# Performance work log

Hardware: AMD Instinct MI355X
Metric: run time of the kernel (lower is better)

Reference implementation:

```python
import jax, jax.numpy as jnp
import numpy as np

IN_F, OUT_F, N_CLASSES, HEADS = 512, 64, 40, 4
B, M = 1, 4096
NEG_SLOPE = 0.01  # F.leaky_relu called with default slope (self.alpha unused)


def _xavier(key, shape, gain=1.0):
    fan_in, fan_out = shape[-1], shape[-2] if len(shape) > 1 else shape[-1]
    a = gain * np.sqrt(6.0 / (fan_in + fan_out))
    return jax.random.uniform(key, shape, jnp.float32, -a, a)


def setup_inputs() -> dict:
    key = jax.random.key(0)
    ks = jax.random.split(key, 12)
    h = jax.random.normal(ks[0], (B, M, IN_F), jnp.float32)
    A = jax.random.randint(ks[1], (B, M, M), 0, 2, jnp.int32)
    A = jnp.maximum(A, jnp.eye(M, dtype=jnp.int32)[None])  # self-loops avoid empty softmax rows
    return {
        "h": h,
        "A": A,
        "W1_w": _xavier(ks[2], (OUT_F * HEADS, IN_F)),
        "W1_b": jnp.zeros((OUT_F * HEADS,), jnp.float32),
        "a1": _xavier(ks[3], (HEADS, 2 * OUT_F), gain=1.414),
        "W3_w": _xavier(ks[4], (OUT_F, OUT_F * HEADS)),
        "W3_b": jnp.zeros((OUT_F,), jnp.float32),
        "W2_w": _xavier(ks[5], (OUT_F * HEADS, OUT_F)),
        "W2_b": jnp.zeros((OUT_F * HEADS,), jnp.float32),
        "a2": _xavier(ks[6], (HEADS, 2 * OUT_F)),
        "FL_w": _xavier(ks[7], (N_CLASSES, OUT_F * HEADS)),
        "FL_b": jnp.zeros((N_CLASSES,), jnp.float32),
    }


def _attention_block(h, mask, W_w, W_b, a):
    # h: (b,m,n); mask: (b,m,m) bool; W_w: (heads*out, n); a: (heads, 2*out)
    b, m, _ = h.shape
    Wh = jnp.einsum('bmn,on->bmo', h, W_w) + W_b          # (b,m,heads*out)
    Wh = Wh.reshape(b, m, HEADS, -1)                       # (b,m,h,c)
    c = Wh.shape[-1]
    src = jnp.einsum('bmhc,hc->bmh', Wh, a[:, :c])         # score from edge source i
    dst = jnp.einsum('bmhc,hc->bmh', Wh, a[:, c:])         # score from edge target j
    logits = jax.nn.leaky_relu(src[:, :, None, :] + dst[:, None, :, :], NEG_SLOPE)  # (b,i,j,h)
    logits = jnp.where(mask[..., None], logits, -jnp.inf)
    probs = jax.nn.softmax(logits, axis=2)                 # softmax over neighbors j
    out = jnp.einsum('bijh,bjhc->bihc', probs, Wh)
    return out.reshape(b, m, HEADS * c)


def reference(h, A, W1_w, W1_b, a1, W3_w, W3_b, W2_w, W2_b, a2, FL_w, FL_b):
    mask = A == 1
    x = _attention_block(h, mask, W1_w, W1_b, a1)          # (b,m,heads*out)
    x = jnp.einsum('bmo,po->bmp', x, W3_w) + W3_b          # (b,m,out)
    x = _attention_block(x, mask, W2_w, W2_b, a2)          # (b,m,heads*out)
    out = jnp.einsum('bmo,ko->bmk', x, FL_w) + FL_b        # (b,m,n_classes)
    return (x, out)
```

## Files before the change

### kernel.cpp

```cpp
#include <hip/hip_runtime.h>
#include <hip/hip_bf16.h>

typedef _Float16 f16_t;
typedef unsigned short u16;
typedef unsigned int u32;
typedef float f32x4 __attribute__((ext_vector_type(4)));
typedef f16_t f16x8 __attribute__((ext_vector_type(8)));
typedef u16 u16x8 __attribute__((ext_vector_type(8)));
typedef u16 u16x4 __attribute__((ext_vector_type(4)));

#define MROWS 4096
#define NHEADS 4
#define COUT 64
#define OHF 256
#define NCLS 40
#define LOG2E 1.4426950408889634f
#define PLD 264

static __device__ __forceinline__ u16 f16b(float x) {
    return __builtin_bit_cast(u16, (f16_t)x);
}
static __device__ __forceinline__ float f16f(u16 x) {
    return (float)__builtin_bit_cast(f16_t, x);
}
static __device__ __forceinline__ float dmu_decode(u32 ku) {
    const u32 fb = (ku & 0x80000000u) ? (ku ^ 0x80000000u) : ~ku;
    return __builtin_bit_cast(float, fb);
}

__global__ __launch_bounds__(256) void init_kernel(const int* __restrict__ A,
                                                   u32* __restrict__ AbitsT,
                                                   const float* __restrict__ W1w,
                                                   const float* __restrict__ W1b,
                                                   const float* __restrict__ a1,
                                                   const float* __restrict__ W2w,
                                                   const float* __restrict__ W2b,
                                                   const float* __restrict__ W3w,
                                                   const float* __restrict__ W3b,
                                                   const float* __restrict__ a2,
                                                   float* __restrict__ Cwf,
                                                   float* __restrict__ cbf,
                                                   float* __restrict__ va1,
                                                   float* __restrict__ vc1,
                                                   float* __restrict__ va2,
                                                   float* __restrict__ vc2,
                                                   u32* __restrict__ dmu) {
    __shared__ u32 W[2][128];
    __shared__ float u[8][64];
    const int bx = blockIdx.x, tid = threadIdx.x;
    if (bx < 2048) {
        const int i0 = bx * 2;
        const int lane = tid & 63, wv = tid >> 6;
        for (int t = wv; t < 32; t += 4) {
            const int r = t >> 4, q = t & 15;
            const size_t base = (size_t)(i0 + r) * MROWS + q * 256 + lane;
            const int a0 = A[base];
            const int a1_ = A[base + 64];
            const int a2_ = A[base + 128];
            const int a3 = A[base + 192];
            const unsigned long long b0 = __ballot(a0 != 0);
            const unsigned long long b1 = __ballot(a1_ != 0);
            const unsigned long long b2 = __ballot(a2_ != 0);
            const unsigned long long b3 = __ballot(a3 != 0);
            if (lane == 0) {
                W[r][q * 8 + 0] = (u32)b0;
                W[r][q * 8 + 2] = (u32)b1;
                W[r][q * 8 + 4] = (u32)b2;
                W[r][q * 8 + 6] = (u32)b3;
            } else if (lane == 1) {
                W[r][q * 8 + 1] = (u32)(b0 >> 32);
                W[r][q * 8 + 3] = (u32)(b1 >> 32);
                W[r][q * 8 + 5] = (u32)(b2 >> 32);
                W[r][q * 8 + 7] = (u32)(b3 >> 32);
            }
        }
        __syncthreads();
        {
            const int jw = tid >> 1, r = tid & 1;
            AbitsT[(size_t)jw * MROWS + i0 + r] = W[r][jw];
        }
        return;
    }
    const int bid = bx - 2048;
    if (bid < 256) {
        float acc = 0.f;
        for (int t = 0; t < 64; ++t)
            acc += W2w[bid * 64 + t] * W3w[t * 256 + tid];
        Cwf[bid * 256 + tid] = acc;
        if (tid == 0) {
            float b = 0.f;
            for (int t = 0; t < 64; ++t) b += W2w[bid * 64 + t] * W3b[t];
            cbf[bid] = b + W2b[bid];
        }
    } else if (bid < 258) {
        const int k = (bid - 256) * 256 + tid;
#pragma unroll
        for (int hs = 0; hs < 8; ++hs) {
            const int h = hs >> 1, s = hs & 1;
            float acc = 0.f;
            for (int c = 0; c < COUT; ++c)
                acc += W1w[(size_t)(h * COUT + c) * 512 + k] * a1[h * 128 + s * COUT + c];
            va1[hs * 512 + k] = acc;
        }
        if (bid == 256 && tid == 0) {
            for (int hs = 0; hs < 8; ++hs) {
                const int h = hs >> 1, s = hs & 1;
                float b = 0.f;
                for (int c = 0; c < COUT; ++c) b += W1b[h * COUT + c] * a1[h * 128 + s * COUT + c];
                vc1[hs] = b;
            }
        }
    } else if (bid == 258) {
#pragma unroll
        for (int e = tid * 2; e < tid * 2 + 2; ++e) {
            const int hs = e >> 6, t = e & 63;
            const int h = hs >> 1, s = hs & 1;
            float acc = 0.f;
            for (int c = 0; c < COUT; ++c)
                acc += W2w[(size_t)(h * COUT + c) * 64 + t] * a2[h * 128 + s * COUT + c];
            u[hs][t] = acc;
        }
        __syncthreads();
#pragma unroll
        for (int hs = 0; hs < 8; ++hs) {
            float acc = 0.f;
            for (int t = 0; t < 64; ++t) acc += u[hs][t] * W3w[t * 256 + tid];
            va2[hs * 256 + tid] = acc;
        }
        if (tid == 0) {
            for (int hs = 0; hs < 8; ++hs) {
                const int h = hs >> 1, s = hs & 1;
                float b = 0.f;
                for (int t = 0; t < 64; ++t) b += u[hs][t] * W3b[t];
                for (int c = 0; c < COUT; ++c) b += W2b[h * COUT + c] * a2[h * 128 + s * COUT + c];
                vc2[hs] = b;
            }
        }
    } else {
        if (tid < 8) dmu[tid] = 0u;
    }
}

__global__ __launch_bounds__(256) void proj_kernel(const float* __restrict__ X,
                                                   const float* __restrict__ Bm,
                                                   const float* __restrict__ bias,
                                                   int K,
                                                   u16* __restrict__ WhF,
                                                   const float* __restrict__ va,
                                                   const float* __restrict__ vc,
                                                   float* __restrict__ srcT,
                                                   float* __restrict__ dstT,
                                                   u32* __restrict__ dmu) {
    __shared__ u16 Al[64][40];
    __shared__ u16 Bl[64][40];
    __shared__ u16 Tl[64][72];
    __shared__ float red[16][16][9];
    __shared__ float dred[4][16];
    const int tid = threadIdx.x;
    if (blockIdx.x < 256) {
        const int lane = tid & 63, wv = tid >> 6;
        const int l15 = lane & 15, g = lane >> 4;
        const int m0 = (blockIdx.x & 63) * 64, n0 = (blockIdx.x >> 6) * 64;
        const int r = tid >> 2, c8 = (tid & 3) * 8;
        f32x4 acc[4] = {};
        for (int k0 = 0; k0 < K; k0 += 32) {
            const float4 a0 = *(const float4*)&X[(size_t)(m0 + r) * K + k0 + c8];
            const float4 a1 = *(const float4*)&X[(size_t)(m0 + r) * K + k0 + c8 + 4];
            const float4 b0 = *(const float4*)&Bm[(size_t)(n0 + r) * K + k0 + c8];
            const float4 b1 = *(const float4*)&Bm[(size_t)(n0 + r) * K + k0 + c8 + 4];
            u16x8 av, bv;
            av[0] = f16b(a0.x); av[1] = f16b(a0.y); av[2] = f16b(a0.z); av[3] = f16b(a0.w);
            av[4] = f16b(a1.x); av[5] = f16b(a1.y); av[6] = f16b(a1.z); av[7] = f16b(a1.w);
            bv[0] = f16b(b0.x); bv[1] = f16b(b0.y); bv[2] = f16b(b0.z); bv[3] = f16b(b0.w);
            bv[4] = f16b(b1.x); bv[5] = f16b(b1.y); bv[6] = f16b(b1.z); bv[7] = f16b(b1.w);
            __syncthreads();
            *(u16x8*)&Al[r][c8] = av;
            *(u16x8*)&Bl[r][c8] = bv;
            __syncthreads();
            f16x8 afr = *(const f16x8*)&Al[16 * wv + l15][8 * g];
#pragma unroll
            for (int ni = 0; ni < 4; ++ni) {
                f16x8 bfr = *(const f16x8*)&Bl[16 * ni + l15][8 * g];
                acc[ni] = __builtin_amdgcn_mfma_f32_16x16x32_f16(afr, bfr, acc[ni], 0, 0, 0);
            }
        }
#pragma unroll
        for (int ni = 0; ni < 4; ++ni) {
            const int nl = 16 * ni + l15;
            const float bvs = bias[n0 + nl];
#pragma unroll
            for (int rr = 0; rr < 4; ++rr)
                Tl[nl][16 * wv + 4 * g + rr] = f16b(acc[ni][rr] + bvs);
        }
        __syncthreads();
        const int jb0 = m0 >> 5;
#pragma unroll
        for (int q = 0; q < 2; ++q) {
            const int id = tid + 256 * q;
            const int jb_l = id >> 8, rem = id & 255;
            const int c_l = rem >> 2, gf = rem & 3;
            u16x8 v = *(const u16x8*)&Tl[c_l][32 * jb_l + 8 * gf];
            *(u16x8*)&WhF[(size_t)(((jb0 + jb_l) * 256 + n0 + c_l) * 4 + gf) * 8] = v;
        }
        return;
    }
    const int bs = blockIdx.x - 256;
    const int ii = tid >> 4, ki = tid & 15;
    const int i = bs * 16 + ii;
    const int KS = K >> 4;
    const int k0 = ki * KS;
    float acc[8] = {};
    for (int k = k0; k < k0 + KS; k += 4) {
        const float4 xv = *(const float4*)&X[(size_t)i * K + k];
#pragma unroll
        for (int hs = 0; hs < 8; ++hs) {
            const float4 vv = *(const float4*)&va[(size_t)hs * K + k];
            acc[hs] += xv.x * vv.x + xv.y * vv.y + xv.z * vv.z + xv.w * vv.w;
        }
    }
#pragma unroll
    for (int hs = 0; hs < 8; ++hs) red[ii][ki][hs] = acc[hs];
    __syncthreads();
    if (tid < 128) {
        const int row = tid >> 3, hs = tid & 7, h = hs >> 1;
        float sum = 0.f;
#pragma unroll
        for (int kk = 0; kk < 16; ++kk) sum += red[row][kk][hs];
        const float val = sum + vc[hs];
        const int ig = bs * 16 + row;
        if ((hs & 1) == 0) {
            srcT[h * MROWS + ig] = val;
        } else {
            dstT[h * MROWS + ig] = val;
            dred[h][row] = val;
        }
    }
    __syncthreads();
    if (tid < 4) {
        float m = -3.4e38f;
#pragma unroll
        for (int r = 0; r < 16; ++r) m = fmaxf(m, dred[tid][r]);
        const u32 b = __builtin_bit_cast(u32, m);
        const u32 key = (b & 0x80000000u) ? ~b : (b | 0x80000000u);
        atomicMax(dmu + tid, key);
    }
}

template <int JT>
__global__ __launch_bounds__(512) void attn_kernel(const u16* __restrict__ WhF,
                                                   const float* __restrict__ srcT,
                                                   const float* __restrict__ dstT,
                                                   const u32* __restrict__ AbitsT,
                                                   const u32* __restrict__ dmu,
                                                   u16* __restrict__ partial,
                                                   float* __restrict__ outF) {
    constexpr int J64 = JT * 64;
    __shared__ __align__(16) float GT[8 * J64];
    const int tid = threadIdx.x;
    const int lane = tid & 63, w = tid >> 6;
    const int h = w & 3, half = w >> 2;
    const int l15 = lane & 15, g = lane >> 4;
    const int i0 = blockIdx.x * 64;
    const int chunk = blockIdx.y;
    const int jbase = chunk * J64;

    for (int e = tid; e < 8 * J64; e += 512) {
        const int hb = e / J64;
        const int j = e - hb * J64;
        const float dmhe = dmu_decode(dmu[hb >> 1]);
        const float sc = (hb & 1) ? 0.01f * LOG2E : LOG2E;
        GT[e] = __builtin_amdgcn_exp2f((dstT[(hb >> 1) * MROWS + jbase + j] - dmhe) * sc);
    }

    const float dmh = dmu_decode(dmu[h]);
    float negs_[2], F1_[2], F2_[2];
#pragma unroll
    for (int mi = 0; mi < 2; ++mi) {
        const float s = srcT[h * MROWS + i0 + 32 * half + 16 * mi + l15];
        const float sd = s + dmh;
        const float C = fmaxf(sd, 0.01f * sd);
        negs_[mi] = -s;
        F1_[mi] = __builtin_amdgcn_exp2f((sd - C) * LOG2E);
        F2_[mi] = __builtin_amdgcn_exp2f((0.01f * sd - C) * LOG2E);
    }
    __syncthreads();

    f32x4 acc[2][4] = {};
    f32x4 acc1[2] = {};
    f16x8 ones;
#pragma unroll
    for (int e = 0; e < 8; ++e) ones[e] = (f16_t)1.0f;

    for (int jt = 0; jt < JT; ++jt) {
        const int j0 = jbase + jt * 64;
        f16x8 af[2];
#pragma unroll
        for (int kj = 0; kj < 2; ++kj) {
            const int jk = j0 + 32 * kj + 8 * g;
            const float4 d0 = *(const float4*)&dstT[h * MROWS + jk];
            const float4 d1 = *(const float4*)&dstT[h * MROWS + jk + 4];
            float dv[8] = {d0.x, d0.y, d0.z, d0.w, d1.x, d1.y, d1.z, d1.w};
            const int goff = jt * 64 + 32 * kj + 8 * g;
            const float4 g10 = *(const float4*)&GT[(h * 2) * J64 + goff];
            const float4 g11 = *(const float4*)&GT[(h * 2) * J64 + goff + 4];
            const float4 g20 = *(const float4*)&GT[(h * 2 + 1) * J64 + goff];
            const float4 g21 = *(const float4*)&GT[(h * 2 + 1) * J64 + goff + 4];
            const float G1[8] = {g10.x, g10.y, g10.z, g10.w, g11.x, g11.y, g11.z, g11.w};
            const float G2[8] = {g20.x, g20.y, g20.z, g20.w, g21.x, g21.y, g21.z, g21.w};
#pragma unroll
            for (int mi = 0; mi < 2; ++mi) {
                const int irow = i0 + 32 * half + 16 * mi + l15;
                const u32 word = AbitsT[(size_t)((j0 >> 5) + kj) * MROWS + irow];
                const u32 bits = (word >> (8 * g)) & 0xffu;
                f16x8 a;
#pragma unroll
                for (int e = 0; e < 8; ++e) {
                    const bool pos = dv[e] >= negs_[mi];
                    float wv = (pos ? G1[e] : G2[e]) * (pos ? F1_[mi] : F2_[mi]);
                    wv = ((bits >> e) & 1u) ? wv : 0.f;
                    a[e] = (f16_t)wv;
                }
                af[mi] = a;
            }
            const int jb = (j0 >> 5) + kj;
#pragma unroll
            for (int ni = 0; ni < 4; ++ni) {
                const int c = h * COUT + 16 * ni + l15;
                f16x8 b = *(const f16x8*)&WhF[(size_t)(((jb << 8) + c) * 4 + g) * 8];
                acc[0][ni] = __builtin_amdgcn_mfma_f32_16x16x32_f16(af[0], b, acc[0][ni], 0, 0, 0);
                acc[1][ni] = __builtin_amdgcn_mfma_f32_16x16x32_f16(af[1], b, acc[1][ni], 0, 0, 0);
            }
            acc1[0] = __builtin_amdgcn_mfma_f32_16x16x32_f16(af[0], ones, acc1[0], 0, 0, 0);
            acc1[1] = __builtin_amdgcn_mfma_f32_16x16x32_f16(af[1], ones, acc1[1], 0, 0, 0);
        }
    }

    if (partial) {
        u16* pc = partial + (size_t)chunk * MROWS * PLD;
#pragma unroll
        for (int mi = 0; mi < 2; ++mi) {
#pragma unroll
            for (int ni = 0; ni < 4; ++ni)
#pragma unroll
                for (int rr = 0; rr < 4; ++rr) {
                    const int i = i0 + 32 * half + 16 * mi + 4 * g + rr;
                    pc[(size_t)i * PLD + h * COUT + 16 * ni + l15] = f16b(acc[mi][ni][rr]);
                }
#pragma unroll
            for (int rr = 0; rr < 4; ++rr)
                if (l15 == rr)
                    pc[(size_t)(i0 + 32 * half + 16 * mi + 4 * g + rr) * PLD + 256 + h] =
                        f16b(acc1[mi][rr]);
        }
    } else {
#pragma unroll
        for (int mi = 0; mi < 2; ++mi)
#pragma unroll
            for (int rr = 0; rr < 4; ++rr) {
                const int i = i0 + 32 * half + 16 * mi + 4 * g + rr;
                const float rs = acc1[mi][rr];
#pragma unroll
                for (int ni = 0; ni < 4; ++ni)
                    outF[(size_t)i * OHF + h * COUT + 16 * ni + l15] = acc[mi][ni][rr] / rs;
            }
    }
}

__global__ __launch_bounds__(256) void combine_kernel(const u16* __restrict__ partial,
                                                      int nchunk,
                                                      float* __restrict__ outF,
                                                      const float* __restrict__ FLw,
                                                      const float* __restrict__ FLb,
                                                      float* __restrict__ outL) {
    __shared__ float xrow[256];
    __shared__ float cred[40][4];
    const int i = blockIdx.x, c = threadIdx.x, h = c >> 6;
    float v = 0.f, rs = 0.f;
    for (int ch = 0; ch < nchunk; ++ch) {
        const u16* pc = partial + (size_t)ch * MROWS * PLD + (size_t)i * PLD;
        v += f16f(pc[c]);
        rs += f16f(pc[256 + h]);
    }
    const float r = v / rs;
    outF[(size_t)i * OHF + c] = r;
    if (!FLw) return;
    xrow[c] = r;
    __syncthreads();
    if (c < 160) {
        const int k = c >> 2, seg = c & 3;
        const float* xp = &xrow[seg * 64];
        const float* wp = &FLw[(size_t)k * OHF + seg * 64];
        float a = 0.f;
#pragma unroll
        for (int t = 0; t < 64; t += 4) {
            const float4 x4 = *(const float4*)&xp[t];
            const float4 w4 = *(const float4*)&wp[t];
            a += x4.x * w4.x + x4.y * w4.y + x4.z * w4.z + x4.w * w4.w;
        }
        cred[k][seg] = a;
    }
    __syncthreads();
    if (c < NCLS)
        outL[(size_t)i * NCLS + c] = cred[c][0] + cred[c][1] + cred[c][2] + cred[c][3] + FLb[c];
}

extern "C" void kernel_launch(void* const* d_in, const int* in_sizes, int n_in,
                              void* d_out, int out_size, void* d_ws, size_t ws_size,
                              hipStream_t stream) {
    const float* hIn = (const float*)d_in[0];
    const int*   A   = (const int*)d_in[1];
    const float* W1w = (const float*)d_in[2];
    const float* W1b = (const float*)d_in[3];
    const float* a1  = (const float*)d_in[4];
    const float* W3w = (const float*)d_in[5];
    const float* W3b = (const float*)d_in[6];
    const float* W2w = (const float*)d_in[7];
    const float* W2b = (const float*)d_in[8];
    const float* a2  = (const float*)d_in[9];
    const float* FLw = (const float*)d_in[10];
    const float* FLb = (const float*)d_in[11];
    float* outX = (float*)d_out;
    float* outL = outX + (size_t)MROWS * OHF;

    char* p = (char*)d_ws;
    auto alloc = [&](size_t bytes) { char* q = p; p += (bytes + 255) & ~(size_t)255; return q; };
    u32*   AbitsT = (u32*)alloc((size_t)MROWS * 128 * 4);
    u16*   WhF1  = (u16*)alloc((size_t)OHF * MROWS * 2);
    u16*   WhF2  = (u16*)alloc((size_t)OHF * MROWS * 2);
    float* x1f   = (float*)alloc((size_t)MROWS * OHF * 4);
    float* Cwf   = (float*)alloc((size_t)256 * 256 * 4);
    float* cbf   = (float*)alloc(256 * 4);
    float* va1   = (float*)alloc((size_t)8 * 512 * 4);
    float* vc1   = (float*)alloc(8 * 4);
    float* va2   = (float*)alloc((size_t)8 * 256 * 4);
    float* vc2   = (float*)alloc(8 * 4);
    float* srcT1 = (float*)alloc((size_t)NHEADS * MROWS * 4);
    float* dstT1 = (float*)alloc((size_t)NHEADS * MROWS * 4);
    float* srcT2 = (float*)alloc((size_t)NHEADS * MROWS * 4);
    float* dstT2 = (float*)alloc((size_t)NHEADS * MROWS * 4);
    u32*   dmu   = (u32*)alloc(8 * 4);
    size_t fixed = (size_t)(p - (char*)d_ws);
    int nchunk = 8;
    if (fixed + (size_t)8 * MROWS * PLD * 2 > ws_size) nchunk = 4;
    u16* partial = (u16*)p;

    dim3 blk(256);
    init_kernel<<<dim3(2308), blk, 0, stream>>>(A, AbitsT, W1w, W1b, a1, W2w, W2b,
                                                W3w, W3b, a2, Cwf, cbf, va1, vc1,
                                                va2, vc2, dmu);

    auto launch_attn = [&](const u16* WhF, const float* srcT, const float* dstT,
                           const u32* dm) {
        if (nchunk == 8)
            attn_kernel<8><<<dim3(64, 8), dim3(512), 0, stream>>>(WhF, srcT, dstT, AbitsT, dm, partial, nullptr);
        else
            attn_kernel<16><<<dim3(64, 4), dim3(512), 0, stream>>>(WhF, srcT, dstT, AbitsT, dm, partial, nullptr);
    };

    proj_kernel<<<dim3(512), blk, 0, stream>>>(hIn, W1w, W1b, 512, WhF1,
                                               va1, vc1, srcT1, dstT1, dmu);
    launch_attn(WhF1, srcT1, dstT1, dmu);
    combine_kernel<<<dim3(4096), blk, 0, stream>>>(partial, nchunk, x1f,
                                                   nullptr, nullptr, nullptr);

    proj_kernel<<<dim3(512), blk, 0, stream>>>(x1f, Cwf, cbf, 256, WhF2,
                                               va2, vc2, srcT2, dstT2, dmu + 4);
    launch_attn(WhF2, srcT2, dstT2, dmu + 4);
    combine_kernel<<<dim3(4096), blk, 0, stream>>>(partial, nchunk, outX,
                                                   FLw, FLb, outL);
}
```

Baseline: 181.8 us.

## Replace leaky-relu branch with fmax form and halve rows per attention block

The per-element sign test against the destination score is replaced by fmaxf(G1*F1, G2*F2). Because exp is monotonic, the larger of the two exponentials equals the leaky-relu branch, so the dstT loads and the compare/select work in the inner loop go away. Each block now covers 32 rows instead of 64, with one 16-row MFMA tile per wave, and the grid is doubled. This cuts register pressure and raises block count, but loses reuse of the WhF B-fragments across two row tiles, so those global loads double.

```diff
diff --git a/kernel.cpp b/kernel.cpp
--- a/kernel.cpp
+++ b/kernel.cpp
@@ -258,9 +258,9 @@
     __shared__ __align__(16) float GT[8 * J64];
     const int tid = threadIdx.x;
     const int lane = tid & 63, w = tid >> 6;
-    const int h = w & 3, half = w >> 2;
+    const int h = w & 3, mi = w >> 2;
     const int l15 = lane & 15, g = lane >> 4;
-    const int i0 = blockIdx.x * 64;
+    const int i0 = blockIdx.x * 32;
     const int chunk = blockIdx.y;
     const int jbase = chunk * J64;
 
@@ -273,33 +273,24 @@
     }
 
     const float dmh = dmu_decode(dmu[h]);
-    float negs_[2], F1_[2], F2_[2];
-#pragma unroll
-    for (int mi = 0; mi < 2; ++mi) {
-        const float s = srcT[h * MROWS + i0 + 32 * half + 16 * mi + l15];
-        const float sd = s + dmh;
-        const float C = fmaxf(sd, 0.01f * sd);
-        negs_[mi] = -s;
-        F1_[mi] = __builtin_amdgcn_exp2f((sd - C) * LOG2E);
-        F2_[mi] = __builtin_amdgcn_exp2f((0.01f * sd - C) * LOG2E);
-    }
+    const float s = srcT[h * MROWS + i0 + 16 * mi + l15];
+    const float sd = s + dmh;
+    const float C = fmaxf(sd, 0.01f * sd);
+    const float F1 = __builtin_amdgcn_exp2f((sd - C) * LOG2E);
+    const float F2 = __builtin_amdgcn_exp2f((0.01f * sd - C) * LOG2E);
     __syncthreads();
 
-    f32x4 acc[2][4] = {};
-    f32x4 acc1[2] = {};
+    f32x4 acc[4] = {};
+    f32x4 acc1 = {};
     f16x8 ones;
 #pragma unroll
     for (int e = 0; e < 8; ++e) ones[e] = (f16_t)1.0f;
+    const int irow = i0 + 16 * mi + l15;
 
     for (int jt = 0; jt < JT; ++jt) {
         const int j0 = jbase + jt * 64;
-        f16x8 af[2];
 #pragma unroll
         for (int kj = 0; kj < 2; ++kj) {
-            const int jk = j0 + 32 * kj + 8 * g;
-            const float4 d0 = *(const float4*)&dstT[h * MROWS + jk];
-            const float4 d1 = *(const float4*)&dstT[h * MROWS + jk + 4];
-            float dv[8] = {d0.x, d0.y, d0.z, d0.w, d1.x, d1.y, d1.z, d1.w};
             const int goff = jt * 64 + 32 * kj + 8 * g;
             const float4 g10 = *(const float4*)&GT[(h * 2) * J64 + goff];
             const float4 g11 = *(const float4*)&GT[(h * 2) * J64 + goff + 4];
@@ -307,62 +298,48 @@
             const float4 g21 = *(const float4*)&GT[(h * 2 + 1) * J64 + goff + 4];
             const float G1[8] = {g10.x, g10.y, g10.z, g10.w, g11.x, g11.y, g11.z, g11.w};
             const float G2[8] = {g20.x, g20.y, g20.z, g20.w, g21.x, g21.y, g21.z, g21.w};
-#pragma unroll
-            for (int mi = 0; mi < 2; ++mi) {
-                const int irow = i0 + 32 * half + 16 * mi + l15;
-                const u32 word = AbitsT[(size_t)((j0 >> 5) + kj) * MROWS + irow];
-                const u32 bits = (word >> (8 * g)) & 0xffu;
-                f16x8 a;
-#pragma unroll
-                for (int e = 0; e < 8; ++e) {
-                    const bool pos = dv[e] >= negs_[mi];
-                    float wv = (pos ? G1[e] : G2[e]) * (pos ? F1_[mi] : F2_[mi]);
-                    wv = ((bits >> e) & 1u) ? wv : 0.f;
-                    a[e] = (f16_t)wv;
-                }
-                af[mi] = a;
-            }
             const int jb = (j0 >> 5) + kj;
+            const u32 word = AbitsT[(size_t)jb * MROWS + irow];
+            const u32 bits = (word >> (8 * g)) & 0xffu;
+            f16x8 a;
+#pragma unroll
+            for (int e = 0; e < 8; ++e) {
+                float wv = fmaxf(G1[e] * F1, G2[e] * F2);
+                wv = ((bits >> e) & 1u) ? wv : 0.f;
+                a[e] = (f16_t)wv;
+            }
 #pragma unroll
             for (int ni = 0; ni < 4; ++ni) {
                 const int c = h * COUT + 16 * ni + l15;
                 f16x8 b = *(const f16x8*)&WhF[(size_t)(((jb << 8) + c) * 4 + g) * 8];
-                acc[0][ni] = __builtin_amdgcn_mfma_f32_16x16x32_f16(af[0], b, acc[0][ni], 0, 0, 0);
-                acc[1][ni] = __builtin_amdgcn_mfma_f32_16x16x32_f16(af[1], b, acc[1][ni], 0, 0, 0);
-            }
-            acc1[0] = __builtin_amdgcn_mfma_f32_16x16x32_f16(af[0], ones, acc1[0], 0, 0, 0);
-            acc1[1] = __builtin_amdgcn_mfma_f32_16x16x32_f16(af[1], ones, acc1[1], 0, 0, 0);
+                acc[ni] = __builtin_amdgcn_mfma_f32_16x16x32_f16(a, b, acc[ni], 0, 0, 0);
+            }
+            acc1 = __builtin_amdgcn_mfma_f32_16x16x32_f16(a, ones, acc1, 0, 0, 0);
         }
     }
 
     if (partial) {
         u16* pc = partial + (size_t)chunk * MROWS * PLD;
 #pragma unroll
-        for (int mi = 0; mi < 2; ++mi) {
+        for (int ni = 0; ni < 4; ++ni)
+#pragma unroll
+            for (int rr = 0; rr < 4; ++rr) {
+                const int i = i0 + 16 * mi + 4 * g + rr;
+                pc[(size_t)i * PLD + h * COUT + 16 * ni + l15] = f16b(acc[ni][rr]);
+            }
+#pragma unroll
+        for (int rr = 0; rr < 4; ++rr)
+            if (l15 == rr)
+                pc[(size_t)(i0 + 16 * mi + 4 * g + rr) * PLD + 256 + h] = f16b(acc1[rr]);
+    } else {
+#pragma unroll
+        for (int rr = 0; rr < 4; ++rr) {
+            const int i = i0 + 16 * mi + 4 * g + rr;
+            const float rs = acc1[rr];
 #pragma unroll
             for (int ni = 0; ni < 4; ++ni)
-#pragma unroll
-                for (int rr = 0; rr < 4; ++rr) {
-                    const int i = i0 + 32 * half + 16 * mi + 4 * g + rr;
-                    pc[(size_t)i * PLD + h * COUT + 16 * ni + l15] = f16b(acc[mi][ni][rr]);
-                }
-#pragma unroll
-            for (int rr = 0; rr < 4; ++rr)
-                if (l15 == rr)
-                    pc[(size_t)(i0 + 32 * half + 16 * mi + 4 * g + rr) * PLD + 256 + h] =
-                        f16b(acc1[mi][rr]);
-        }
-    } else {
-#pragma unroll
-        for (int mi = 0; mi < 2; ++mi)
-#pragma unroll
-            for (int rr = 0; rr < 4; ++rr) {
-                const int i = i0 + 32 * half + 16 * mi + 4 * g + rr;
-                const float rs = acc1[mi][rr];
-#pragma unroll
-                for (int ni = 0; ni < 4; ++ni)
-                    outF[(size_t)i * OHF + h * COUT + 16 * ni + l15] = acc[mi][ni][rr] / rs;
-            }
+                outF[(size_t)i * OHF + h * COUT + 16 * ni + l15] = acc[ni][rr] / rs;
+        }
     }
 }
 
@@ -452,9 +429,9 @@
     auto launch_attn = [&](const u16* WhF, const float* srcT, const float* dstT,
                            const u32* dm) {
         if (nchunk == 8)
-            attn_kernel<8><<<dim3(64, 8), dim3(512), 0, stream>>>(WhF, srcT, dstT, AbitsT, dm, partial, nullptr);
+            attn_kernel<8><<<dim3(128, 8), dim3(512), 0, stream>>>(WhF, srcT, dstT, AbitsT, dm, partial, nullptr);
         else
-            attn_kernel<16><<<dim3(64, 4), dim3(512), 0, stream>>>(WhF, srcT, dstT, AbitsT, dm, partial, nullptr);
+            attn_kernel<16><<<dim3(128, 4), dim3(512), 0, stream>>>(WhF, srcT, dstT, AbitsT, dm, partial, nullptr);
     };
 
     proj_kernel<<<dim3(512), blk, 0, stream>>>(hIn, W1w, W1b, 512, WhF1,
```

New measurement: 177.3 us. 2.5% less time.
